# Kernel tuning notes

Measured on AMD Instinct MI355X. Metric: run time of the kernel, lower is better.

Reference implementation:

```python
import jax, jax.numpy as jnp
import numpy as np

LN_EPS = 1e-5

def setup_inputs() -> dict:
    key = jax.random.key(0)
    ks = jax.random.split(key, 6)
    T, S, H = 1024, 128, 512
    text_embeds = jax.random.normal(ks[0], (T, H), dtype=jnp.float32)
    struct_embeds = jax.random.normal(ks[1], (S, H), dtype=jnp.float32)
    mask = jax.random.randint(ks[2], (T, S), 0, 2, dtype=jnp.int32)
    # gate_linear: Linear(2H, H), xavier_uniform weight, zero bias
    limit = float(np.sqrt(6.0 / (2 * H + H)))
    gate_w = jax.random.uniform(ks[3], (H, 2 * H), minval=-limit, maxval=limit, dtype=jnp.float32)
    gate_b = jnp.zeros((H,), dtype=jnp.float32)
    ln_gamma = jnp.ones((H,), dtype=jnp.float32)
    ln_beta = jnp.zeros((H,), dtype=jnp.float32)
    return {"text_embeds": text_embeds, "struct_embeds": struct_embeds, "mask": mask,
            "gate_w": gate_w, "gate_b": gate_b, "ln_gamma": ln_gamma, "ln_beta": ln_beta}

def _layernorm(x, gamma, beta):
    mu = jnp.mean(x, axis=-1, keepdims=True)
    var = jnp.mean(jnp.square(x - mu), axis=-1, keepdims=True)
    return (x - mu) * jax.lax.rsqrt(var + LN_EPS) * gamma + beta

def reference(text_embeds, struct_embeds, mask, gate_w, gate_b, ln_gamma, ln_beta):
    H = text_embeds.shape[-1]
    # Linear on concat([text, struct]) == text @ Wt.T + struct @ Ws.T + b (same math, no [T,S,2H] concat)
    wt, ws = gate_w[:, :H], gate_w[:, H:]          # each [H, H]
    gt = text_embeds @ wt.T                        # [T, H]
    gs = struct_embeds @ ws.T                      # [S, H]
    gates = jax.nn.relu(gt[:, None, :] + gs[None, :, :] + gate_b)  # [T, S, H]
    gates = gates * mask.astype(gates.dtype)[:, :, None]           # masked gates
    enrichment = jnp.einsum('tsh,sh->th', gates, struct_embeds)    # weighted sum over struct
    enriched = _layernorm(text_embeds + enrichment, ln_gamma, ln_beta)
    return (enriched, gates)
```

## Files before the change

### kernel.cpp

```cpp
#include <hip/hip_runtime.h>
#include <hip/hip_bf16.h>

#define TT 1024
#define SS 128
#define HH 512
#define LN_EPS 1e-5f

__global__ __launch_bounds__(256) void proj_gemm(
    const float* __restrict__ text, const float* __restrict__ structe,
    const float* __restrict__ gate_w, float* __restrict__ P,
    float* __restrict__ gsb)
{
    const int bz = blockIdx.z;
    const int bm = blockIdx.x;
    const int bn = blockIdx.y;

    const float* A;
    int off, k_begin, k_len;
    float* C;
    if (bz < 4) {
        A = text + bm * 64 * HH;
        off = 0;
        k_begin = bz * 128;
        k_len = 128;
        C = P + (size_t)bz * (TT * HH) + bm * 64 * HH + bn * 64;
    } else {
        if (bm >= 2) return;
        A = structe + bm * 64 * HH;
        off = HH;
        k_begin = 0;
        k_len = HH;
        C = gsb + bm * 64 * HH + bn * 64;
    }
    const int n_base = bn * 64;

    __shared__ float As[16][68];
    __shared__ float Bs[16][68];

    const int tid  = threadIdx.x;
    const int lrow = tid >> 2;
    const int lc   = tid & 3;
    const int ty   = tid >> 4;
    const int tx   = tid & 15;

    float acc[4][4] = {};

    const float* a_ptr = A + lrow * HH + k_begin + lc * 4;
    const float* b_ptr = gate_w + (size_t)(n_base + lrow) * (2 * HH) + off + k_begin + lc * 4;

    for (int k = 0; k < k_len; k += 16) {
        float4 av = *(const float4*)a_ptr;  a_ptr += 16;
        float4 bv = *(const float4*)b_ptr;  b_ptr += 16;
        __syncthreads();
        As[lc * 4 + 0][lrow] = av.x; As[lc * 4 + 1][lrow] = av.y;
        As[lc * 4 + 2][lrow] = av.z; As[lc * 4 + 3][lrow] = av.w;
        Bs[lc * 4 + 0][lrow] = bv.x; Bs[lc * 4 + 1][lrow] = bv.y;
        Bs[lc * 4 + 2][lrow] = bv.z; Bs[lc * 4 + 3][lrow] = bv.w;
        __syncthreads();
        #pragma unroll
        for (int kk = 0; kk < 16; ++kk) {
            float4 a4 = *(const float4*)&As[kk][ty * 4];
            float4 b4 = *(const float4*)&Bs[kk][tx * 4];
            float a[4] = {a4.x, a4.y, a4.z, a4.w};
            float b[4] = {b4.x, b4.y, b4.z, b4.w};
            #pragma unroll
            for (int i = 0; i < 4; ++i)
                #pragma unroll
                for (int j = 0; j < 4; ++j)
                    acc[i][j] = fmaf(a[i], b[j], acc[i][j]);
        }
    }

    #pragma unroll
    for (int i = 0; i < 4; ++i) {
        float4 v = make_float4(acc[i][0], acc[i][1], acc[i][2], acc[i][3]);
        *(float4*)(C + (size_t)(ty * 4 + i) * HH + tx * 4) = v;
    }
}

__global__ __launch_bounds__(256) void fuse_k(
    const float* __restrict__ text, const float* __restrict__ structe,
    const int* __restrict__ mask, const float* __restrict__ gate_b,
    const float* __restrict__ P, const float* __restrict__ gsb,
    const float* __restrict__ gamma, const float* __restrict__ beta,
    float* __restrict__ enriched, float* __restrict__ gates)
{
    const int t   = blockIdx.x;
    const int tid = threadIdx.x;
    const int lh  = tid & 127;
    const int sg  = tid >> 7;
    const int h4  = lh * 4;

    __shared__ int msk[SS];
    if (tid < SS) msk[tid] = mask[t * SS + tid];

    float4 p0 = *(const float4*)(P + (size_t)0 * TT * HH + (size_t)t * HH + h4);
    float4 p1 = *(const float4*)(P + (size_t)1 * TT * HH + (size_t)t * HH + h4);
    float4 p2 = *(const float4*)(P + (size_t)2 * TT * HH + (size_t)t * HH + h4);
    float4 p3 = *(const float4*)(P + (size_t)3 * TT * HH + (size_t)t * HH + h4);
    float4 gb = *(const float4*)(gate_b + h4);
    float4 gt4;
    gt4.x = p0.x + p1.x + p2.x + p3.x + gb.x;
    gt4.y = p0.y + p1.y + p2.y + p3.y + gb.y;
    gt4.z = p0.z + p1.z + p2.z + p3.z + gb.z;
    gt4.w = p0.w + p1.w + p2.w + p3.w + gb.w;

    __syncthreads();

    float4 acc = make_float4(0.f, 0.f, 0.f, 0.f);
    const int s_begin = sg * 64;

    const float* gs_ptr = gsb     + (size_t)s_begin * HH + h4;
    const float* sv_ptr = structe + (size_t)s_begin * HH + h4;
    float*       g_ptr  = gates + ((size_t)t * SS + s_begin) * HH + h4;

    #pragma unroll 4
    for (int si = 0; si < 64; ++si) {
        float4 gs4 = *(const float4*)gs_ptr;  gs_ptr += HH;
        float4 sv  = *(const float4*)sv_ptr;  sv_ptr += HH;
        const float mk = (float)msk[s_begin + si];
        float4 g;
        g.x = fmaxf(gt4.x + gs4.x, 0.f) * mk;
        g.y = fmaxf(gt4.y + gs4.y, 0.f) * mk;
        g.z = fmaxf(gt4.z + gs4.z, 0.f) * mk;
        g.w = fmaxf(gt4.w + gs4.w, 0.f) * mk;
        *(float4*)g_ptr = g;  g_ptr += HH;
        acc.x = fmaf(g.x, sv.x, acc.x);
        acc.y = fmaf(g.y, sv.y, acc.y);
        acc.z = fmaf(g.z, sv.z, acc.z);
        acc.w = fmaf(g.w, sv.w, acc.w);
    }

    __shared__ float accs[HH];
    if (sg) *(float4*)&accs[h4] = acc;
    __syncthreads();

    float x0 = 0.f, x1 = 0.f, x2 = 0.f, x3 = 0.f;
    float s1 = 0.f, s2 = 0.f;
    if (!sg) {
        float4 o  = *(float4*)&accs[h4];
        float4 tv = *(const float4*)(text + (size_t)t * HH + h4);
        x0 = tv.x + acc.x + o.x;
        x1 = tv.y + acc.y + o.y;
        x2 = tv.z + acc.z + o.z;
        x3 = tv.w + acc.w + o.w;
        s1 = x0 + x1 + x2 + x3;
        s2 = x0 * x0 + x1 * x1 + x2 * x2 + x3 * x3;
    }
    #pragma unroll
    for (int o = 32; o; o >>= 1) {
        s1 += __shfl_down(s1, o);
        s2 += __shfl_down(s2, o);
    }
    __shared__ float red[8];
    if ((tid & 63) == 0) { red[tid >> 6] = s1; red[4 + (tid >> 6)] = s2; }
    __syncthreads();
    const float sum = red[0] + red[1] + red[2] + red[3];
    const float ssq = red[4] + red[5] + red[6] + red[7];
    const float mu   = sum * (1.0f / HH);
    const float var  = ssq * (1.0f / HH) - mu * mu;
    const float rstd = rsqrtf(var + LN_EPS);

    if (!sg) {
        float4 gm = *(const float4*)(gamma + h4);
        float4 bt = *(const float4*)(beta + h4);
        float4 o;
        o.x = (x0 - mu) * rstd * gm.x + bt.x;
        o.y = (x1 - mu) * rstd * gm.y + bt.y;
        o.z = (x2 - mu) * rstd * gm.z + bt.z;
        o.w = (x3 - mu) * rstd * gm.w + bt.w;
        *(float4*)(enriched + (size_t)t * HH + h4) = o;
    }
}

extern "C" void kernel_launch(void* const* d_in, const int* in_sizes, int n_in,
                              void* d_out, int out_size, void* d_ws, size_t ws_size,
                              hipStream_t stream) {
    const float* text    = (const float*)d_in[0];
    const float* structe = (const float*)d_in[1];
    const int*   mask    = (const int*)d_in[2];
    const float* gate_w  = (const float*)d_in[3];
    const float* gate_b  = (const float*)d_in[4];
    const float* gamma   = (const float*)d_in[5];
    const float* beta    = (const float*)d_in[6];

    float* out      = (float*)d_out;
    float* enriched = out;
    float* gates    = out + (size_t)TT * HH;

    float* P   = (float*)d_ws;
    float* gsb = P + (size_t)4 * TT * HH;

    proj_gemm<<<dim3(16, 8, 5), 256, 0, stream>>>(text, structe, gate_w, P, gsb);
    fuse_k<<<TT, 256, 0, stream>>>(text, structe, mask, gate_b, P, gsb,
                                   gamma, beta, enriched, gates);
}
```

Baseline: 318.3 us.

## Process four text rows per 1024-thread block with eight struct groups

```diff
diff --git a/kernel.cpp b/kernel.cpp
--- a/kernel.cpp
+++ b/kernel.cpp
@@ -78,98 +78,109 @@
     }
 }
 
-__global__ __launch_bounds__(256) void fuse_k(
+__global__ __launch_bounds__(1024) void fuse_k(
     const float* __restrict__ text, const float* __restrict__ structe,
     const int* __restrict__ mask, const float* __restrict__ gate_b,
     const float* __restrict__ P, const float* __restrict__ gsb,
     const float* __restrict__ gamma, const float* __restrict__ beta,
     float* __restrict__ enriched, float* __restrict__ gates)
 {
-    const int t   = blockIdx.x;
+    const int t0  = blockIdx.x * 4;
     const int tid = threadIdx.x;
     const int lh  = tid & 127;
     const int sg  = tid >> 7;
     const int h4  = lh * 4;
 
-    __shared__ int msk[SS];
-    if (tid < SS) msk[tid] = mask[t * SS + tid];
-
-    float4 p0 = *(const float4*)(P + (size_t)0 * TT * HH + (size_t)t * HH + h4);
-    float4 p1 = *(const float4*)(P + (size_t)1 * TT * HH + (size_t)t * HH + h4);
-    float4 p2 = *(const float4*)(P + (size_t)2 * TT * HH + (size_t)t * HH + h4);
-    float4 p3 = *(const float4*)(P + (size_t)3 * TT * HH + (size_t)t * HH + h4);
-    float4 gb = *(const float4*)(gate_b + h4);
-    float4 gt4;
-    gt4.x = p0.x + p1.x + p2.x + p3.x + gb.x;
-    gt4.y = p0.y + p1.y + p2.y + p3.y + gb.y;
-    gt4.z = p0.z + p1.z + p2.z + p3.z + gb.z;
-    gt4.w = p0.w + p1.w + p2.w + p3.w + gb.w;
+    __shared__ int   msk[4 * SS];
+    __shared__ float accs[8][HH];
+    __shared__ float red[2], red2[2];
+
+    if (tid < 4 * SS) msk[tid] = mask[t0 * SS + tid];
+
+    const float4 gb = *(const float4*)(gate_b + h4);
+    const int s_begin = sg * 16;
 
     __syncthreads();
 
-    float4 acc = make_float4(0.f, 0.f, 0.f, 0.f);
-    const int s_begin = sg * 64;
-
-    const float* gs_ptr = gsb     + (size_t)s_begin * HH + h4;
-    const float* sv_ptr = structe + (size_t)s_begin * HH + h4;
-    float*       g_ptr  = gates + ((size_t)t * SS + s_begin) * HH + h4;
-
-    #pragma unroll 4
-    for (int si = 0; si < 64; ++si) {
-        float4 gs4 = *(const float4*)gs_ptr;  gs_ptr += HH;
-        float4 sv  = *(const float4*)sv_ptr;  sv_ptr += HH;
-        const float mk = (float)msk[s_begin + si];
-        float4 g;
-        g.x = fmaxf(gt4.x + gs4.x, 0.f) * mk;
-        g.y = fmaxf(gt4.y + gs4.y, 0.f) * mk;
-        g.z = fmaxf(gt4.z + gs4.z, 0.f) * mk;
-        g.w = fmaxf(gt4.w + gs4.w, 0.f) * mk;
-        *(float4*)g_ptr = g;  g_ptr += HH;
-        acc.x = fmaf(g.x, sv.x, acc.x);
-        acc.y = fmaf(g.y, sv.y, acc.y);
-        acc.z = fmaf(g.z, sv.z, acc.z);
-        acc.w = fmaf(g.w, sv.w, acc.w);
-    }
-
-    __shared__ float accs[HH];
-    if (sg) *(float4*)&accs[h4] = acc;
-    __syncthreads();
-
-    float x0 = 0.f, x1 = 0.f, x2 = 0.f, x3 = 0.f;
-    float s1 = 0.f, s2 = 0.f;
-    if (!sg) {
-        float4 o  = *(float4*)&accs[h4];
-        float4 tv = *(const float4*)(text + (size_t)t * HH + h4);
-        x0 = tv.x + acc.x + o.x;
-        x1 = tv.y + acc.y + o.y;
-        x2 = tv.z + acc.z + o.z;
-        x3 = tv.w + acc.w + o.w;
-        s1 = x0 + x1 + x2 + x3;
-        s2 = x0 * x0 + x1 * x1 + x2 * x2 + x3 * x3;
-    }
-    #pragma unroll
-    for (int o = 32; o; o >>= 1) {
-        s1 += __shfl_down(s1, o);
-        s2 += __shfl_down(s2, o);
-    }
-    __shared__ float red[8];
-    if ((tid & 63) == 0) { red[tid >> 6] = s1; red[4 + (tid >> 6)] = s2; }
-    __syncthreads();
-    const float sum = red[0] + red[1] + red[2] + red[3];
-    const float ssq = red[4] + red[5] + red[6] + red[7];
-    const float mu   = sum * (1.0f / HH);
-    const float var  = ssq * (1.0f / HH) - mu * mu;
-    const float rstd = rsqrtf(var + LN_EPS);
-
-    if (!sg) {
-        float4 gm = *(const float4*)(gamma + h4);
-        float4 bt = *(const float4*)(beta + h4);
-        float4 o;
-        o.x = (x0 - mu) * rstd * gm.x + bt.x;
-        o.y = (x1 - mu) * rstd * gm.y + bt.y;
-        o.z = (x2 - mu) * rstd * gm.z + bt.z;
-        o.w = (x3 - mu) * rstd * gm.w + bt.w;
-        *(float4*)(enriched + (size_t)t * HH + h4) = o;
+    for (int tt = 0; tt < 4; ++tt) {
+        const int t = t0 + tt;
+
+        float4 p0 = *(const float4*)(P + (size_t)0 * TT * HH + (size_t)t * HH + h4);
+        float4 p1 = *(const float4*)(P + (size_t)1 * TT * HH + (size_t)t * HH + h4);
+        float4 p2 = *(const float4*)(P + (size_t)2 * TT * HH + (size_t)t * HH + h4);
+        float4 p3 = *(const float4*)(P + (size_t)3 * TT * HH + (size_t)t * HH + h4);
+        float4 gt4;
+        gt4.x = p0.x + p1.x + p2.x + p3.x + gb.x;
+        gt4.y = p0.y + p1.y + p2.y + p3.y + gb.y;
+        gt4.z = p0.z + p1.z + p2.z + p3.z + gb.z;
+        gt4.w = p0.w + p1.w + p2.w + p3.w + gb.w;
+
+        float4 acc = make_float4(0.f, 0.f, 0.f, 0.f);
+
+        const float* gs_ptr = gsb     + (size_t)s_begin * HH + h4;
+        const float* sv_ptr = structe + (size_t)s_begin * HH + h4;
+        float*       g_ptr  = gates + ((size_t)t * SS + s_begin) * HH + h4;
+        const int*   mrow   = msk + tt * SS + s_begin;
+
+        #pragma unroll 8
+        for (int si = 0; si < 16; ++si) {
+            float4 gs4 = *(const float4*)gs_ptr;  gs_ptr += HH;
+            float4 sv  = *(const float4*)sv_ptr;  sv_ptr += HH;
+            const float mk = (float)mrow[si];
+            float4 g;
+            g.x = fmaxf(gt4.x + gs4.x, 0.f) * mk;
+            g.y = fmaxf(gt4.y + gs4.y, 0.f) * mk;
+            g.z = fmaxf(gt4.z + gs4.z, 0.f) * mk;
+            g.w = fmaxf(gt4.w + gs4.w, 0.f) * mk;
+            *(float4*)g_ptr = g;  g_ptr += HH;
+            acc.x = fmaf(g.x, sv.x, acc.x);
+            acc.y = fmaf(g.y, sv.y, acc.y);
+            acc.z = fmaf(g.z, sv.z, acc.z);
+            acc.w = fmaf(g.w, sv.w, acc.w);
+        }
+
+        *(float4*)&accs[sg][h4] = acc;
+        __syncthreads();
+
+        float x0 = 0.f, x1 = 0.f, x2 = 0.f, x3 = 0.f;
+        if (sg == 0) {
+            float4 a = acc;
+            #pragma unroll
+            for (int q = 1; q < 8; ++q) {
+                float4 o = *(float4*)&accs[q][h4];
+                a.x += o.x; a.y += o.y; a.z += o.z; a.w += o.w;
+            }
+            float4 tv = *(const float4*)(text + (size_t)t * HH + h4);
+            x0 = tv.x + a.x;
+            x1 = tv.y + a.y;
+            x2 = tv.z + a.z;
+            x3 = tv.w + a.w;
+            float s1 = x0 + x1 + x2 + x3;
+            float s2 = x0 * x0 + x1 * x1 + x2 * x2 + x3 * x3;
+            #pragma unroll
+            for (int o = 32; o; o >>= 1) {
+                s1 += __shfl_down(s1, o);
+                s2 += __shfl_down(s2, o);
+            }
+            if ((tid & 63) == 0) { red[tid >> 6] = s1; red2[tid >> 6] = s2; }
+        }
+        __syncthreads();
+
+        if (sg == 0) {
+            const float sum = red[0] + red[1];
+            const float ssq = red2[0] + red2[1];
+            const float mu   = sum * (1.0f / HH);
+            const float var  = ssq * (1.0f / HH) - mu * mu;
+            const float rstd = rsqrtf(var + LN_EPS);
+            float4 gm = *(const float4*)(gamma + h4);
+            float4 bt = *(const float4*)(beta + h4);
+            float4 o;
+            o.x = (x0 - mu) * rstd * gm.x + bt.x;
+            o.y = (x1 - mu) * rstd * gm.y + bt.y;
+            o.z = (x2 - mu) * rstd * gm.z + bt.z;
+            o.w = (x3 - mu) * rstd * gm.w + bt.w;
+            *(float4*)(enriched + (size_t)t * HH + h4) = o;
+        }
     }
 }
 
@@ -192,6 +203,6 @@
     float* gsb = P + (size_t)4 * TT * HH;
 
     proj_gemm<<<dim3(16, 8, 5), 256, 0, stream>>>(text, structe, gate_w, P, gsb);
-    fuse_k<<<TT, 256, 0, stream>>>(text, structe, mask, gate_b, P, gsb,
-                                   gamma, beta, enriched, gates);
+    fuse_k<<<256, 1024, 0, stream>>>(text, structe, mask, gate_b, P, gsb,
+                                     gamma, beta, enriched, gates);
 }
```

Measured after the change: 320.0 us. Within noise of the previous version (+0.5%).
